# Optimization experiments

Hardware: AMD Instinct MI355X
Metric: run time of the kernel (lower is better)

Reference implementation:

```python
import jax, jax.numpy as jnp
import numpy as np

R_SCALE = 0.2
CHUNK = 32


def setup_inputs() -> dict:
    key = jax.random.key(0)
    ks = jax.random.split(key, 7)
    N, P, T = 262144, 256, 8
    return {
        "coord": jax.random.normal(ks[0], (N, 3), dtype=jnp.float32),
        "particle_pos": jax.random.normal(ks[1], (P, T, 3), dtype=jnp.float32),
        "particle_dir": jax.random.normal(ks[2], (P, T, 3), dtype=jnp.float32),
        "particle_intensity": jax.random.uniform(ks[3], (P, T, 1), dtype=jnp.float32),
        "intensity_raw": jax.random.uniform(ks[4], (P, 1), dtype=jnp.float32),
        "radius_u": jax.random.uniform(ks[5], (P, 1), dtype=jnp.float32),
        "time_mask": jax.random.randint(ks[6], (P, T), 0, 2, dtype=jnp.int32),
        "time_idx": 3,
    }


def _confinement(coord, pos, dirs, inten, r):
    # coord: [N,3]; pos/dirs: [P,3]; inten/r: [P,1]. Chunked all-pairs reduce.
    P = pos.shape[0]
    nc = P // CHUNK
    pos_c = pos.reshape(nc, CHUNK, 3)
    dir_c = dirs.reshape(nc, CHUNK, 3)
    int_c = inten.reshape(nc, CHUNK, 1)
    r_c = r.reshape(nc, CHUNK, 1)

    def body(acc, inp):
        p, d, w, rr = inp  # [c,3],[c,3],[c,1],[c,1]
        rr = rr[:, :, None]  # [c,1,1]
        loc = p[:, None, :] - coord[None]            # [c,N,3]
        dist = jnp.linalg.norm(loc, axis=-1, keepdims=True)  # [c,N,1]
        locn = loc / dist
        infl = jnp.exp(-dist ** 2 / (2 * rr ** 2)) / (rr ** 3 * 40000)
        infl = infl * (dist < 3 * rr).astype(coord.dtype)
        vort = infl * d[:, None, :]                  # [c,N,3]
        each = w[:, None, :] * jnp.cross(locn, vort) # [c,N,3]
        return acc + each.sum(axis=0), None

    acc0 = jnp.zeros_like(coord)
    acc, _ = jax.lax.scan(body, acc0, (pos_c, dir_c, int_c, r_c))
    return acc


def reference(coord, particle_pos, particle_dir, particle_intensity,
              intensity_raw, radius_u, time_mask, time_idx):
    pos = particle_pos[:, time_idx]            # [P,3]
    dirs = particle_dir[:, time_idx]           # [P,3]
    mask = time_mask[:, time_idx].astype(coord.dtype)[:, None]  # [P,1]
    inten = jnp.sqrt(jnp.clip(intensity_raw, 0.0, 10.0) + 1e-8)
    inten = inten * particle_intensity[:, time_idx] * mask      # [P,1]
    r = jax.nn.relu(R_SCALE * (0.5 * radius_u + 1.0))           # [P,1]
    return _confinement(coord, pos, dirs, inten, r)
```

## Files before the change

### kernel.cpp

```cpp
#include <hip/hip_runtime.h>

#define THREADS 256
#define CPT     4
#define NPMAX   256

typedef __attribute__((ext_vector_type(2))) float f32x2;

static __device__ __forceinline__ f32x2 v2(float v) { f32x2 r; r.x = v; r.y = v; return r; }
static __device__ __forceinline__ f32x2 fmav(f32x2 a, f32x2 b, f32x2 c) {
    return __builtin_elementwise_fma(a, b, c);
}

#define INTER4(pa, pb) { \
    { \
        f32x2 lx = v2(pa.x) - cxA, ly = v2(pa.y) - cyA, lz = v2(pa.z) - czA; \
        f32x2 d2 = fmav(lx, lx, fmav(ly, ly, lz * lz)); \
        f32x2 arg = d2 * v2(pa.w); \
        f32x2 s; \
        s.x = __builtin_amdgcn_exp2f(arg.x) * __builtin_amdgcn_rsqf(d2.x); \
        s.y = __builtin_amdgcn_exp2f(arg.y) * __builtin_amdgcn_rsqf(d2.y); \
        s.x = (d2.x < pb.w) ? s.x : 0.0f; \
        s.y = (d2.y < pb.w) ? s.y : 0.0f; \
        f32x2 crx = fmav(ly, v2(pb.z), -(lz * v2(pb.y))); \
        f32x2 cry = fmav(lz, v2(pb.x), -(lx * v2(pb.z))); \
        f32x2 crz = fmav(lx, v2(pb.y), -(ly * v2(pb.x))); \
        axA = fmav(s, crx, axA); ayA = fmav(s, cry, ayA); azA = fmav(s, crz, azA); \
    } \
    { \
        f32x2 lx = v2(pa.x) - cxB, ly = v2(pa.y) - cyB, lz = v2(pa.z) - czB; \
        f32x2 d2 = fmav(lx, lx, fmav(ly, ly, lz * lz)); \
        f32x2 arg = d2 * v2(pa.w); \
        f32x2 s; \
        s.x = __builtin_amdgcn_exp2f(arg.x) * __builtin_amdgcn_rsqf(d2.x); \
        s.y = __builtin_amdgcn_exp2f(arg.y) * __builtin_amdgcn_rsqf(d2.y); \
        s.x = (d2.x < pb.w) ? s.x : 0.0f; \
        s.y = (d2.y < pb.w) ? s.y : 0.0f; \
        f32x2 crx = fmav(ly, v2(pb.z), -(lz * v2(pb.y))); \
        f32x2 cry = fmav(lz, v2(pb.x), -(lx * v2(pb.z))); \
        f32x2 crz = fmav(lx, v2(pb.y), -(ly * v2(pb.x))); \
        axB = fmav(s, crx, axB); ayB = fmav(s, cry, ayB); azB = fmav(s, crz, azB); \
    } \
}

__global__ __launch_bounds__(THREADS) void vortex_fused(
        const float* __restrict__ coord,
        const float* __restrict__ ppos,
        const float* __restrict__ pdir,
        const float* __restrict__ pint,
        const float* __restrict__ iraw,
        const float* __restrict__ rad,
        const int*   __restrict__ tmask,
        const int*   __restrict__ tidxp,
        float*       __restrict__ out,
        int N, int P, int T) {
    __shared__ float4 sp[2 * NPMAX + 4];
    __shared__ int    wtot[THREADS / 64];
    __shared__ int    s_cnt;

    const int tid  = threadIdx.x;
    const int lane = tid & 63;
    const int wid  = tid >> 6;

    const int i0 = blockIdx.x * (THREADS * CPT) + tid;
    const int i1 = i0 + THREADS;
    const int i2 = i0 + 2 * THREADS;
    const int i3 = i0 + 3 * THREADS;
    const bool v0 = (i0 < N), v1 = (i1 < N), v2_ = (i2 < N), v3 = (i3 < N);
    f32x2 cxA = v2(0.f), cyA = v2(0.f), czA = v2(0.f);
    f32x2 cxB = v2(0.f), cyB = v2(0.f), czB = v2(0.f);
    if (v0) { cxA.x = coord[3 * i0]; cyA.x = coord[3 * i0 + 1]; czA.x = coord[3 * i0 + 2]; }
    if (v1) { cxA.y = coord[3 * i1]; cyA.y = coord[3 * i1 + 1]; czA.y = coord[3 * i1 + 2]; }
    if (v2_) { cxB.x = coord[3 * i2]; cyB.x = coord[3 * i2 + 1]; czB.x = coord[3 * i2 + 2]; }
    if (v3) { cxB.y = coord[3 * i3]; cyB.y = coord[3 * i3 + 1]; czB.y = coord[3 * i3 + 2]; }

    const int t = *tidxp;
    bool active = false;
    float4 a, b;
    if (tid < P) {
        const int p = tid;
        float m  = (float)tmask[p * T + t];
        float cl = fminf(fmaxf(iraw[p], 0.0f), 10.0f);
        float w  = sqrtf(cl + 1e-8f) * pint[p * T + t] * m;
        float r  = fmaxf(0.2f * (0.5f * rad[p] + 1.0f), 0.0f);
        active   = (w != 0.0f) && (r > 0.0f);
        if (active) {
            const float* pp = ppos + (size_t)(p * T + t) * 3;
            const float* pd = pdir + (size_t)(p * T + t) * 3;
            float A = w / (r * r * r * 40000.0f);
            a = make_float4(pp[0], pp[1], pp[2], -1.442695040888963f / (2.0f * r * r));
            b = make_float4(A * pd[0], A * pd[1], A * pd[2], 9.0f * r * r);
        }
    }
    unsigned long long bm = __ballot(active);
    int pre = __popcll(bm & ((1ull << lane) - 1ull));
    if (lane == 0) wtot[wid] = __popcll(bm);
    __syncthreads();
    int off = 0, tot = 0;
    #pragma unroll
    for (int w2 = 0; w2 < THREADS / 64; ++w2) {
        int c = wtot[w2];
        if (w2 < wid) off += c;
        tot += c;
    }
    if (active) {
        int pos = off + pre;
        sp[2 * pos]     = a;
        sp[2 * pos + 1] = b;
    }
    const int tot_pad = (tot + 1) & ~1;
    if (tid >= tot && tid < tot_pad) {
        float4 z = make_float4(0.f, 0.f, 0.f, 0.f);
        sp[2 * tid]     = z;
        sp[2 * tid + 1] = z;
    }
    if (tid == 0) s_cnt = tot_pad;
    __syncthreads();
    const int cnt = s_cnt;

    f32x2 axA = v2(0.f), ayA = v2(0.f), azA = v2(0.f);
    f32x2 axB = v2(0.f), ayB = v2(0.f), azB = v2(0.f);

    float4 pa0 = sp[0], pb0 = sp[1], pa1 = sp[2], pb1 = sp[3];
    for (int p = 0; p < cnt; p += 2) {
        const int q = (p + 2 < cnt) ? (p + 2) : 0;
        float4 na0 = sp[2 * q];
        float4 nb0 = sp[2 * q + 1];
        float4 na1 = sp[2 * q + 2];
        float4 nb1 = sp[2 * q + 3];
        INTER4(pa0, pb0);
        INTER4(pa1, pb1);
        pa0 = na0; pb0 = nb0; pa1 = na1; pb1 = nb1;
    }

    if (v0) { out[3 * i0] = axA.x; out[3 * i0 + 1] = ayA.x; out[3 * i0 + 2] = azA.x; }
    if (v1) { out[3 * i1] = axA.y; out[3 * i1 + 1] = ayA.y; out[3 * i1 + 2] = azA.y; }
    if (v2_) { out[3 * i2] = axB.x; out[3 * i2 + 1] = ayB.x; out[3 * i2 + 2] = azB.x; }
    if (v3) { out[3 * i3] = axB.y; out[3 * i3 + 1] = ayB.y; out[3 * i3 + 2] = azB.y; }
}

extern "C" void kernel_launch(void* const* d_in, const int* in_sizes, int n_in,
                              void* d_out, int out_size, void* d_ws, size_t ws_size,
                              hipStream_t stream) {
    const float* coord = (const float*)d_in[0];
    const float* ppos  = (const float*)d_in[1];
    const float* pdir  = (const float*)d_in[2];
    const float* pint  = (const float*)d_in[3];
    const float* iraw  = (const float*)d_in[4];
    const float* rad   = (const float*)d_in[5];
    const int*   tmask = (const int*)d_in[6];
    const int*   tidx  = (const int*)d_in[7];
    float* out = (float*)d_out;

    const int N = in_sizes[0] / 3;
    const int P = in_sizes[4];
    const int T = in_sizes[3] / P;

    const int coordsPerBlock = THREADS * CPT;
    const int blocks = (N + coordsPerBlock - 1) / coordsPerBlock;
    hipLaunchKernelGGL(vortex_fused, dim3(blocks), dim3(THREADS), 0, stream,
                       coord, ppos, pdir, pint, iraw, rad, tmask, tidx, out, N, P, T);
}
```

Before: 25.87 us.

## Split particle prep into separate kernel and stream particles via uniform global loads

Particle preprocessing and compaction move out of the main kernel into a single-block prep kernel that writes the packed particle list and its count to workspace. The main kernel then reads particles straight from global memory with a wave-uniform count, so the loads can become scalar loads, and it no longer needs LDS, barriers or a software prefetch. This removes the redundant per-block prep and the shared-memory staging. In exchange it adds a second kernel launch with a serial dependency, and the padding grows to a multiple of 8 so the loop can unroll by 8.

```diff
diff --git a/kernel.cpp b/kernel.cpp
--- a/kernel.cpp
+++ b/kernel.cpp
@@ -2,7 +2,7 @@
 
 #define THREADS 256
 #define CPT     4
-#define NPMAX   256
+#define NPMAX   264
 
 typedef __attribute__((ext_vector_type(2))) float f32x2;
 
@@ -42,8 +42,7 @@
     } \
 }
 
-__global__ __launch_bounds__(THREADS) void vortex_fused(
-        const float* __restrict__ coord,
+__global__ __launch_bounds__(THREADS) void vortex_prep(
         const float* __restrict__ ppos,
         const float* __restrict__ pdir,
         const float* __restrict__ pint,
@@ -51,29 +50,15 @@
         const float* __restrict__ rad,
         const int*   __restrict__ tmask,
         const int*   __restrict__ tidxp,
-        float*       __restrict__ out,
-        int N, int P, int T) {
-    __shared__ float4 sp[2 * NPMAX + 4];
-    __shared__ int    wtot[THREADS / 64];
-    __shared__ int    s_cnt;
-
+        int P, int T,
+        float4* __restrict__ parts,
+        int*    __restrict__ dcount) {
+    __shared__ int wtot[THREADS / 64];
     const int tid  = threadIdx.x;
     const int lane = tid & 63;
     const int wid  = tid >> 6;
+    const int t = *tidxp;
 
-    const int i0 = blockIdx.x * (THREADS * CPT) + tid;
-    const int i1 = i0 + THREADS;
-    const int i2 = i0 + 2 * THREADS;
-    const int i3 = i0 + 3 * THREADS;
-    const bool v0 = (i0 < N), v1 = (i1 < N), v2_ = (i2 < N), v3 = (i3 < N);
-    f32x2 cxA = v2(0.f), cyA = v2(0.f), czA = v2(0.f);
-    f32x2 cxB = v2(0.f), cyB = v2(0.f), czB = v2(0.f);
-    if (v0) { cxA.x = coord[3 * i0]; cyA.x = coord[3 * i0 + 1]; czA.x = coord[3 * i0 + 2]; }
-    if (v1) { cxA.y = coord[3 * i1]; cyA.y = coord[3 * i1 + 1]; czA.y = coord[3 * i1 + 2]; }
-    if (v2_) { cxB.x = coord[3 * i2]; cyB.x = coord[3 * i2 + 1]; czB.x = coord[3 * i2 + 2]; }
-    if (v3) { cxB.y = coord[3 * i3]; cyB.y = coord[3 * i3 + 1]; czB.y = coord[3 * i3 + 2]; }
-
-    const int t = *tidxp;
     bool active = false;
     float4 a, b;
     if (tid < P) {
@@ -104,32 +89,47 @@
     }
     if (active) {
         int pos = off + pre;
-        sp[2 * pos]     = a;
-        sp[2 * pos + 1] = b;
+        parts[2 * pos]     = a;
+        parts[2 * pos + 1] = b;
     }
-    const int tot_pad = (tot + 1) & ~1;
+    const int tot_pad = (tot + 7) & ~7;
     if (tid >= tot && tid < tot_pad) {
         float4 z = make_float4(0.f, 0.f, 0.f, 0.f);
-        sp[2 * tid]     = z;
-        sp[2 * tid + 1] = z;
+        parts[2 * tid]     = z;
+        parts[2 * tid + 1] = z;
     }
-    if (tid == 0) s_cnt = tot_pad;
-    __syncthreads();
-    const int cnt = s_cnt;
+    if (tid == 0) *dcount = tot_pad;
+}
+
+__global__ __launch_bounds__(THREADS) void vortex_main(
+        const float*  __restrict__ coord,
+        const float4* __restrict__ parts,
+        const int*    __restrict__ dcount,
+        float*        __restrict__ out,
+        int N) {
+    const int tid = threadIdx.x;
+    const int i0 = blockIdx.x * (THREADS * CPT) + tid;
+    const int i1 = i0 + THREADS;
+    const int i2 = i0 + 2 * THREADS;
+    const int i3 = i0 + 3 * THREADS;
+    const bool v0 = (i0 < N), v1 = (i1 < N), v2_ = (i2 < N), v3 = (i3 < N);
+    f32x2 cxA = v2(0.f), cyA = v2(0.f), czA = v2(0.f);
+    f32x2 cxB = v2(0.f), cyB = v2(0.f), czB = v2(0.f);
+    if (v0) { cxA.x = coord[3 * i0]; cyA.x = coord[3 * i0 + 1]; czA.x = coord[3 * i0 + 2]; }
+    if (v1) { cxA.y = coord[3 * i1]; cyA.y = coord[3 * i1 + 1]; czA.y = coord[3 * i1 + 2]; }
+    if (v2_) { cxB.x = coord[3 * i2]; cyB.x = coord[3 * i2 + 1]; czB.x = coord[3 * i2 + 2]; }
+    if (v3) { cxB.y = coord[3 * i3]; cyB.y = coord[3 * i3 + 1]; czB.y = coord[3 * i3 + 2]; }
+
+    const int cnt = __builtin_amdgcn_readfirstlane(*dcount);
 
     f32x2 axA = v2(0.f), ayA = v2(0.f), azA = v2(0.f);
     f32x2 axB = v2(0.f), ayB = v2(0.f), azB = v2(0.f);
 
-    float4 pa0 = sp[0], pb0 = sp[1], pa1 = sp[2], pb1 = sp[3];
-    for (int p = 0; p < cnt; p += 2) {
-        const int q = (p + 2 < cnt) ? (p + 2) : 0;
-        float4 na0 = sp[2 * q];
-        float4 nb0 = sp[2 * q + 1];
-        float4 na1 = sp[2 * q + 2];
-        float4 nb1 = sp[2 * q + 3];
-        INTER4(pa0, pb0);
-        INTER4(pa1, pb1);
-        pa0 = na0; pb0 = nb0; pa1 = na1; pb1 = nb1;
+    #pragma unroll 8
+    for (int p = 0; p < cnt; ++p) {
+        const float4 pa = parts[2 * p];
+        const float4 pb = parts[2 * p + 1];
+        INTER4(pa, pb);
     }
 
     if (v0) { out[3 * i0] = axA.x; out[3 * i0 + 1] = ayA.x; out[3 * i0 + 2] = azA.x; }
@@ -155,8 +155,14 @@
     const int P = in_sizes[4];
     const int T = in_sizes[3] / P;
 
+    float4* parts = (float4*)d_ws;
+    int* dcount   = (int*)((char*)d_ws + (size_t)2 * NPMAX * sizeof(float4));
+
+    hipLaunchKernelGGL(vortex_prep, dim3(1), dim3(THREADS), 0, stream,
+                       ppos, pdir, pint, iraw, rad, tmask, tidx, P, T, parts, dcount);
+
     const int coordsPerBlock = THREADS * CPT;
     const int blocks = (N + coordsPerBlock - 1) / coordsPerBlock;
-    hipLaunchKernelGGL(vortex_fused, dim3(blocks), dim3(THREADS), 0, stream,
-                       coord, ppos, pdir, pint, iraw, rad, tmask, tidx, out, N, P, T);
+    hipLaunchKernelGGL(vortex_main, dim3(blocks), dim3(THREADS), 0, stream,
+                       coord, parts, dcount, out, N);
 }
```

After: 46.63 us. 80.3% more time.

## Split particle loop across two block teams and merge partial sums

Applied to the files above, without the earlier changes.

Launches the main kernel with a second grid dimension so each coordinate chunk is handled by two blocks, each summing half of the active particles into a separate workspace buffer. A second vectorised kernel then adds the two buffers into the output. The goal is more blocks in flight, since N/1024 = 256 blocks is only about one per CU on this GPU. The cost is a second launch, extra global traffic for the partial buffers, duplicated particle setup per block, and a simpler loop without the explicit LDS prefetch.

```diff
diff --git a/kernel.cpp b/kernel.cpp
--- a/kernel.cpp
+++ b/kernel.cpp
@@ -42,7 +42,7 @@
     } \
 }
 
-__global__ __launch_bounds__(THREADS) void vortex_fused(
+__global__ __launch_bounds__(THREADS) void vortex_team(
         const float* __restrict__ coord,
         const float* __restrict__ ppos,
         const float* __restrict__ pdir,
@@ -51,15 +51,17 @@
         const float* __restrict__ rad,
         const int*   __restrict__ tmask,
         const int*   __restrict__ tidxp,
-        float*       __restrict__ out,
+        float*       __restrict__ bufA,
+        float*       __restrict__ bufB,
         int N, int P, int T) {
-    __shared__ float4 sp[2 * NPMAX + 4];
+    __shared__ float4 sp[2 * NPMAX];
     __shared__ int    wtot[THREADS / 64];
     __shared__ int    s_cnt;
 
     const int tid  = threadIdx.x;
     const int lane = tid & 63;
     const int wid  = tid >> 6;
+    const int team = blockIdx.y;
 
     const int i0 = blockIdx.x * (THREADS * CPT) + tid;
     const int i1 = i0 + THREADS;
@@ -107,35 +109,43 @@
         sp[2 * pos]     = a;
         sp[2 * pos + 1] = b;
     }
-    const int tot_pad = (tot + 1) & ~1;
-    if (tid >= tot && tid < tot_pad) {
-        float4 z = make_float4(0.f, 0.f, 0.f, 0.f);
-        sp[2 * tid]     = z;
-        sp[2 * tid + 1] = z;
-    }
-    if (tid == 0) s_cnt = tot_pad;
+    if (tid == 0) s_cnt = tot;
     __syncthreads();
     const int cnt = s_cnt;
+    const int h   = (cnt + 1) >> 1;
+    const int p0  = team ? h : 0;
+    const int p1  = team ? cnt : h;
 
     f32x2 axA = v2(0.f), ayA = v2(0.f), azA = v2(0.f);
     f32x2 axB = v2(0.f), ayB = v2(0.f), azB = v2(0.f);
-
-    float4 pa0 = sp[0], pb0 = sp[1], pa1 = sp[2], pb1 = sp[3];
-    for (int p = 0; p < cnt; p += 2) {
-        const int q = (p + 2 < cnt) ? (p + 2) : 0;
-        float4 na0 = sp[2 * q];
-        float4 nb0 = sp[2 * q + 1];
-        float4 na1 = sp[2 * q + 2];
-        float4 nb1 = sp[2 * q + 3];
-        INTER4(pa0, pb0);
-        INTER4(pa1, pb1);
-        pa0 = na0; pb0 = nb0; pa1 = na1; pb1 = nb1;
+    #pragma unroll 4
+    for (int p = p0; p < p1; ++p) {
+        const float4 pa = sp[2 * p];
+        const float4 pb = sp[2 * p + 1];
+        INTER4(pa, pb);
     }
 
-    if (v0) { out[3 * i0] = axA.x; out[3 * i0 + 1] = ayA.x; out[3 * i0 + 2] = azA.x; }
-    if (v1) { out[3 * i1] = axA.y; out[3 * i1 + 1] = ayA.y; out[3 * i1 + 2] = azA.y; }
-    if (v2_) { out[3 * i2] = axB.x; out[3 * i2 + 1] = ayB.x; out[3 * i2 + 2] = azB.x; }
-    if (v3) { out[3 * i3] = axB.y; out[3 * i3 + 1] = ayB.y; out[3 * i3 + 2] = azB.y; }
+    float* buf = team ? bufB : bufA;
+    if (v0) { buf[3 * i0] = axA.x; buf[3 * i0 + 1] = ayA.x; buf[3 * i0 + 2] = azA.x; }
+    if (v1) { buf[3 * i1] = axA.y; buf[3 * i1 + 1] = ayA.y; buf[3 * i1 + 2] = azA.y; }
+    if (v2_) { buf[3 * i2] = axB.x; buf[3 * i2 + 1] = ayB.x; buf[3 * i2 + 2] = azB.x; }
+    if (v3) { buf[3 * i3] = axB.y; buf[3 * i3 + 1] = ayB.y; buf[3 * i3 + 2] = azB.y; }
+}
+
+__global__ __launch_bounds__(THREADS) void vortex_merge(
+        const float* __restrict__ bufA,
+        const float* __restrict__ bufB,
+        float* __restrict__ out, int total) {
+    const int i = blockIdx.x * THREADS + threadIdx.x;
+    const int q = total >> 2;
+    if (i < q) {
+        float4 va = ((const float4*)bufA)[i];
+        float4 vb = ((const float4*)bufB)[i];
+        ((float4*)out)[i] = make_float4(va.x + vb.x, va.y + vb.y,
+                                        va.z + vb.z, va.w + vb.w);
+    }
+    const int r = (q << 2) + i;
+    if (i < (total & 3)) out[r] = bufA[r] + bufB[r];
 }
 
 extern "C" void kernel_launch(void* const* d_in, const int* in_sizes, int n_in,
@@ -155,8 +165,16 @@
     const int P = in_sizes[4];
     const int T = in_sizes[3] / P;
 
-    const int coordsPerBlock = THREADS * CPT;
-    const int blocks = (N + coordsPerBlock - 1) / coordsPerBlock;
-    hipLaunchKernelGGL(vortex_fused, dim3(blocks), dim3(THREADS), 0, stream,
-                       coord, ppos, pdir, pint, iraw, rad, tmask, tidx, out, N, P, T);
+    float* bufA = (float*)d_ws;
+    float* bufB = (float*)((char*)d_ws + (size_t)(4 << 20));
+
+    const int chunks = (N + THREADS * CPT - 1) / (THREADS * CPT);
+    hipLaunchKernelGGL(vortex_team, dim3(chunks, 2), dim3(THREADS), 0, stream,
+                       coord, ppos, pdir, pint, iraw, rad, tmask, tidx,
+                       bufA, bufB, N, P, T);
+
+    const int total = 3 * N;
+    const int mblocks = (total / 4 + THREADS - 1) / THREADS;
+    hipLaunchKernelGGL(vortex_merge, dim3(mblocks), dim3(THREADS), 0, stream,
+                       bufA, bufB, out, total);
 }
```

Result: slower. 26.96 us (+4.2%).
